# Kernel tuning notes

Measured on AMD Instinct MI355X. Metric: run time of the kernel, lower is better.

The kernel has to match this reference:

```python
import jax, jax.numpy as jnp
import numpy as np

B, NQ, NK = 4, 2048, 2048
DQ = DK = DV = 256
H = 8
HD = DV // H
EPS = 1e-5


def _ln(x, g, b):
    m = jnp.mean(x, axis=-1, keepdims=True)
    v = jnp.mean(jnp.square(x - m), axis=-1, keepdims=True)
    return (x - m) * jax.lax.rsqrt(v + EPS) * g + b


def setup_inputs() -> dict:
    key = jax.random.key(0)
    ks = jax.random.split(key, 12)
    s = 0.02
    return {
        "Q": jax.random.normal(ks[0], (B, NQ, DQ), jnp.float32),
        "K": jax.random.normal(ks[1], (B, NK, DK), jnp.float32),
        "Wq": jax.random.normal(ks[2], (DV, DQ), jnp.float32) * s,
        "bq": jnp.zeros((DV,), jnp.float32),
        "Wk": jax.random.normal(ks[3], (DV, DK), jnp.float32) * s,
        "bk": jnp.zeros((DV,), jnp.float32),
        "Wv": jax.random.normal(ks[4], (DV, DK), jnp.float32) * s,
        "bv": jnp.zeros((DV,), jnp.float32),
        "Wo": jax.random.normal(ks[5], (DV, DV), jnp.float32) * s,
        "bo": jnp.zeros((DV,), jnp.float32),
        "g0": jnp.ones((DV,), jnp.float32),
        "b0": jnp.zeros((DV,), jnp.float32),
        "g1": jnp.ones((DV,), jnp.float32),
        "b1": jnp.zeros((DV,), jnp.float32),
    }


def reference(Q, K, Wq, bq, Wk, bk, Wv, bv, Wo, bo, g0, b0, g1, b1):
    Qp = Q @ Wq.T + bq            # [B,NQ,DV]
    Kp = K @ Wk.T + bk            # [B,NK,DV]
    Vp = K @ Wv.T + bv            # [B,NK,DV]
    # split(head_dim, dim=2) + cat(dim=0) == reshape heads from contiguous channel chunks
    qh = Qp.reshape(B, NQ, H, HD)
    kh = Kp.reshape(B, NK, H, HD)
    vh = Vp.reshape(B, NK, H, HD)
    scores = jnp.einsum("bqhd,bkhd->bhqk", qh, kh) / jnp.sqrt(jnp.float32(HD))
    attn = jax.nn.softmax(scores, axis=-1)          # [B,H,NQ,NK]
    o = jnp.einsum("bhqk,bkhd->bqhd", attn, vh).reshape(B, NQ, DV)
    o = _ln(o, g0, b0)
    out = o + jax.nn.relu(o @ Wo.T + bo)
    out = _ln(out, g1, b1)
    return out
```

## Files before the change

kernel.cpp:

```cpp
#include <hip/hip_runtime.h>
#include <hip/hip_bf16.h>
#include <math.h>

#define DV 256
#define NH 8
#define NB 4
#define NQ 2048
#define NKK 2048

typedef __attribute__((ext_vector_type(8))) short s8v;
typedef __attribute__((ext_vector_type(16))) float fx16;

typedef const __attribute__((address_space(1))) char g1c;
typedef __attribute__((address_space(3))) char l3c;

__device__ __forceinline__ void gl_lds16(const void* g, void* l) {
    __builtin_amdgcn_global_load_lds((g1c*)g, (l3c*)l, 16, 0, 0);
}
__device__ __forceinline__ unsigned cvtpk_bf16(float lo, float hi) {
    unsigned r;
    asm("v_cvt_pk_bf16_f32 %0, %1, %2" : "=v"(r) : "v"(lo), "v"(hi));
    return r;
}
__device__ __forceinline__ ushort f2bf(float x) {
    unsigned u = __builtin_bit_cast(unsigned, x);
    return (ushort)((u + 0x7fffu + ((u >> 16) & 1u)) >> 16);
}
__device__ __forceinline__ float bf2f(ushort h) {
    return __builtin_bit_cast(float, (unsigned)h << 16);
}

__global__ __launch_bounds__(256) void prep_w_k(
    const float* __restrict__ Wq, const float* __restrict__ Wk,
    const float* __restrict__ Wv, const float* __restrict__ Wo,
    ushort* __restrict__ Wf)
{
    const int j = blockIdx.x * 256 + threadIdx.x;
    const int w = j >> 13, c = j & 8191;
    const int bn = c >> 11, s = (c >> 8) & 7, cc = c & 255;
    const int colblk = cc >> 7, ks = (cc >> 6) & 1, g5w = (cc >> 5) & 1, l31w = cc & 31;
    const int col = bn * 64 + colblk * 32 + l31w;
    const int k = s * 32 + ks * 16 + g5w * 8;
    const float* Wsrc = (w == 0) ? Wq : (w == 1) ? Wk : (w == 2) ? Wv : Wo;
    const float* src = Wsrc + (size_t)col * 256 + k;
    float4 a = *(const float4*)src;
    float4 b = *(const float4*)(src + 4);
    uint4 pk;
    pk.x = cvtpk_bf16(a.x, a.y); pk.y = cvtpk_bf16(a.z, a.w);
    pk.z = cvtpk_bf16(b.x, b.y); pk.w = cvtpk_bf16(b.z, b.w);
    *(uint4*)(Wf + (size_t)j * 8) = pk;
}

__global__ __launch_bounds__(256) void gemm_qkv_k(
    const float* __restrict__ Qf, const float* __restrict__ Kf,
    const ushort* __restrict__ Wf,
    const float* __restrict__ bq, const float* __restrict__ bk, const float* __restrict__ bv,
    ushort* __restrict__ Qb, ushort* __restrict__ Kb, ushort* __restrict__ Vt)
{
    __shared__ __align__(16) char lds[2][20480];
    const int t = threadIdx.x, lane = t & 63, wv = t >> 6;
    const int l31 = lane & 31, g5 = lane >> 5;
    const int bm = blockIdx.x, bn = blockIdx.y;
    const int z = blockIdx.z;
    const float* Af = (z == 0) ? Qf : Kf;
    const ushort* WF = Wf + (size_t)z * 65536;
    const float* bias = (z == 0) ? bq : (z == 1) ? bk : bv;

    int arow[4], aoff[4];
#pragma unroll
    for (int k = 0; k < 4; ++k) {
        const int q = k * 256 + t, c = q >> 1, p = q & 1;
        arow[k] = bm * 128 + (c >> 7) * 32 + (c & 31);
        aoff[k] = ((c >> 6) & 1) * 16 + ((c >> 5) & 1) * 8 + p * 4;
    }
    const ushort* wsrc = WF + (size_t)(bn * 8) * 2048 + t * 8;

#pragma unroll
    for (int k = 0; k < 4; ++k)
        gl_lds16(Af + (size_t)arow[k] * 256 + aoff[k],
                 &lds[0][k * 4096 + wv * 1024 + lane * 16]);
    gl_lds16(wsrc, &lds[0][16384 + wv * 1024 + lane * 16]);
    __syncthreads();

    fx16 acc0 = {}, acc1 = {};
    for (int s = 0; s < 8; ++s) {
        const int buf = s & 1;
        if (s + 1 < 8) {
#pragma unroll
            for (int k = 0; k < 4; ++k)
                gl_lds16(Af + (size_t)arow[k] * 256 + (s + 1) * 32 + aoff[k],
                         &lds[buf ^ 1][k * 4096 + wv * 1024 + lane * 16]);
            gl_lds16(wsrc + (s + 1) * 2048, &lds[buf ^ 1][16384 + wv * 1024 + lane * 16]);
        }
        const char* Al = lds[buf];
        const char* Wl = lds[buf] + 16384;
        float4 fa0 = *(const float4*)(Al + (wv * 2 + 0) * 2048 + lane * 32);
        float4 fb0 = *(const float4*)(Al + (wv * 2 + 0) * 2048 + lane * 32 + 16);
        float4 fa1 = *(const float4*)(Al + (wv * 2 + 1) * 2048 + lane * 32);
        float4 fb1 = *(const float4*)(Al + (wv * 2 + 1) * 2048 + lane * 32 + 16);
        union { unsigned u[4]; s8v v; } A0, A1;
        A0.u[0] = cvtpk_bf16(fa0.x, fa0.y); A0.u[1] = cvtpk_bf16(fa0.z, fa0.w);
        A0.u[2] = cvtpk_bf16(fb0.x, fb0.y); A0.u[3] = cvtpk_bf16(fb0.z, fb0.w);
        A1.u[0] = cvtpk_bf16(fa1.x, fa1.y); A1.u[1] = cvtpk_bf16(fa1.z, fa1.w);
        A1.u[2] = cvtpk_bf16(fb1.x, fb1.y); A1.u[3] = cvtpk_bf16(fb1.z, fb1.w);
        s8v b00 = *(const s8v*)(Wl + 0 * 1024 + lane * 16);
        s8v b01 = *(const s8v*)(Wl + 1 * 1024 + lane * 16);
        s8v b10 = *(const s8v*)(Wl + 2 * 1024 + lane * 16);
        s8v b11 = *(const s8v*)(Wl + 3 * 1024 + lane * 16);
        __builtin_amdgcn_s_setprio(1);
        acc0 = __builtin_amdgcn_mfma_f32_32x32x16_bf16(A0.v, b00, acc0, 0, 0, 0);
        acc0 = __builtin_amdgcn_mfma_f32_32x32x16_bf16(A1.v, b01, acc0, 0, 0, 0);
        acc1 = __builtin_amdgcn_mfma_f32_32x32x16_bf16(A0.v, b10, acc1, 0, 0, 0);
        acc1 = __builtin_amdgcn_mfma_f32_32x32x16_bf16(A1.v, b11, acc1, 0, 0, 0);
        __builtin_amdgcn_s_setprio(0);
        __syncthreads();
    }

    const int row_b = bm * 128 + wv * 32;
    const float CE = 0.17677669529663687f * 1.4426950408889634f;
    const float bs0 = bias[bn * 64 + l31];
    const float bs1 = bias[bn * 64 + 32 + l31];
    if (z == 0) {
#pragma unroll
        for (int r = 0; r < 16; ++r) {
            const int row_g = row_b + (r & 3) + 8 * (r >> 2) + 4 * g5;
            Qb[(size_t)row_g * 256 + bn * 64 + l31]      = f2bf((acc0[r] + bs0) * CE);
            Qb[(size_t)row_g * 256 + bn * 64 + 32 + l31] = f2bf((acc1[r] + bs1) * CE);
        }
    } else if (z == 1) {
#pragma unroll
        for (int r = 0; r < 16; ++r) {
            const int row_g = row_b + (r & 3) + 8 * (r >> 2) + 4 * g5;
            Kb[(size_t)row_g * 256 + bn * 64 + l31]      = f2bf(acc0[r] + bs0);
            Kb[(size_t)row_g * 256 + bn * 64 + 32 + l31] = f2bf(acc1[r] + bs1);
        }
    } else {
#pragma unroll
        for (int r = 0; r < 16; ++r) {
            const int row_g = row_b + (r & 3) + 8 * (r >> 2) + 4 * g5;
            const int bb = row_g >> 11, n = row_g & 2047;
            Vt[((size_t)(bb * 8 + bn * 2 + 0) * 32 + l31) * 2048 + n] = f2bf(acc0[r] + bs0);
            Vt[((size_t)(bb * 8 + bn * 2 + 1) * 32 + l31) * 2048 + n] = f2bf(acc1[r] + bs1);
        }
    }
}

__global__ __launch_bounds__(256) void flash_mfma_k(
    const ushort* __restrict__ Qb, const ushort* __restrict__ Kb,
    const ushort* __restrict__ Vt, ushort* __restrict__ Osb, float* __restrict__ L)
{
    __shared__ __align__(16) char lds[2][8192];
    const int t = threadIdx.x;
    const int lane = t & 63, wv = t >> 6;
    const int l31 = lane & 31, g5 = lane >> 5;
    const int qt = blockIdx.x, h = blockIdx.y;
    const int b = blockIdx.z >> 1, sp = blockIdx.z & 1;

    s8v qf0, qf1;
    {
        const ushort* qp = Qb + (((size_t)b * NQ + qt * 128 + wv * 32 + l31) << 8) + h * 32 + g5 * 8;
        qf0 = *(const s8v*)(qp);
        qf1 = *(const s8v*)(qp + 16);
    }
    s8v ones;
#pragma unroll
    for (int j = 0; j < 8; ++j) ones[j] = (short)0x3F80;

    const ushort* ksrc = Kb + (((size_t)b * NKK + sp * 1024 + ((t >> 7) * 32 + (t & 31))) << 8)
                            + h * 32 + ((t >> 6) & 1) * 16 + ((t >> 5) & 1) * 8;
    const ushort* vsrc = Vt + (((size_t)(b * NH + h) * 32 + (t & 31)) << 11) + sp * 1024
                            + (t >> 6) * 16 + ((t >> 5) & 1) * 8;

    fx16 O0 = {}, lsum = {};

    gl_lds16(ksrc, &lds[0][wv * 1024]);
    gl_lds16(vsrc, &lds[0][4096 + wv * 1024]);
    __syncthreads();

    for (int kt = 0; kt < 16; ++kt) {
        const int buf = kt & 1;
        if (kt + 1 < 16) {
            gl_lds16(ksrc + (size_t)(kt + 1) * 64 * DV, &lds[buf ^ 1][wv * 1024]);
            gl_lds16(vsrc + (kt + 1) * 64, &lds[buf ^ 1][4096 + wv * 1024]);
        }
        const char* Kl = lds[buf];
        const char* Vl = lds[buf] + 4096;
        s8v kf00 = *(const s8v*)(Kl + 0 * 1024 + lane * 16);
        s8v kf01 = *(const s8v*)(Kl + 1 * 1024 + lane * 16);
        s8v kf10 = *(const s8v*)(Kl + 2 * 1024 + lane * 16);
        s8v kf11 = *(const s8v*)(Kl + 3 * 1024 + lane * 16);
        s8v vfa[4];
        vfa[0] = *(const s8v*)(Vl + 0 * 1024 + lane * 16);
        vfa[1] = *(const s8v*)(Vl + 1 * 1024 + lane * 16);
        vfa[2] = *(const s8v*)(Vl + 2 * 1024 + lane * 16);
        vfa[3] = *(const s8v*)(Vl + 3 * 1024 + lane * 16);

        fx16 z = {};
        __builtin_amdgcn_s_setprio(1);
        fx16 Sa = __builtin_amdgcn_mfma_f32_32x32x16_bf16(kf00, qf0, z, 0, 0, 0);
        Sa = __builtin_amdgcn_mfma_f32_32x32x16_bf16(kf01, qf1, Sa, 0, 0, 0);
        fx16 Sb = __builtin_amdgcn_mfma_f32_32x32x16_bf16(kf10, qf0, z, 0, 0, 0);
        Sb = __builtin_amdgcn_mfma_f32_32x32x16_bf16(kf11, qf1, Sb, 0, 0, 0);
        __builtin_amdgcn_s_setprio(0);

        float p[32];
#pragma unroll
        for (int i = 0; i < 16; ++i) {
            p[i]      = __builtin_amdgcn_exp2f(Sa[i]);
            p[16 + i] = __builtin_amdgcn_exp2f(Sb[i]);
        }

        __builtin_amdgcn_s_setprio(1);
#pragma unroll
        for (int kt2 = 0; kt2 < 4; ++kt2) {
            const int pb = 8 * kt2;
            auto ra = __builtin_amdgcn_permlane32_swap(
                cvtpk_bf16(p[pb + 0], p[pb + 1]), cvtpk_bf16(p[pb + 4], p[pb + 5]), false, false);
            auto rb = __builtin_amdgcn_permlane32_swap(
                cvtpk_bf16(p[pb + 2], p[pb + 3]), cvtpk_bf16(p[pb + 6], p[pb + 7]), false, false);
            union { unsigned u[4]; s8v v; } pf;
            pf.u[0] = ra[0]; pf.u[1] = rb[0]; pf.u[2] = ra[1]; pf.u[3] = rb[1];
            O0   = __builtin_amdgcn_mfma_f32_32x32x16_bf16(vfa[kt2], pf.v, O0, 0, 0, 0);
            lsum = __builtin_amdgcn_mfma_f32_32x32x16_bf16(ones,    pf.v, lsum, 0, 0, 0);
        }
        __builtin_amdgcn_s_setprio(0);
        __syncthreads();
    }

    {
        const int qrow = qt * 128 + wv * 32 + l31;
        ushort* dst0 = Osb + (size_t)sp * (8192 * 256)
                     + (((size_t)b * NQ + qrow) << 8) + h * 32 + g5 * 4;
#pragma unroll
        for (int rr = 0; rr < 4; ++rr) {
            uint2 w;
            w.x = cvtpk_bf16(O0[4 * rr + 0], O0[4 * rr + 1]);
            w.y = cvtpk_bf16(O0[4 * rr + 2], O0[4 * rr + 3]);
            *(uint2*)(dst0 + 8 * rr) = w;
        }
        if (g5 == 0)
            L[(((size_t)sp * NB + b) * NH + h) * NQ + qrow] = lsum[0];
    }
}

__global__ __launch_bounds__(256) void tail_fused_k(
    const ushort* __restrict__ Osb, const float* __restrict__ L,
    const ushort* __restrict__ Wfo,
    const float* __restrict__ g0, const float* __restrict__ b0,
    const float* __restrict__ bo, const float* __restrict__ g1,
    const float* __restrict__ b1, float* __restrict__ out)
{
    __shared__ __align__(16) char alds[16384];
    __shared__ __align__(16) char wlds[2][16384];
    __shared__ float red[4][32][2];
    __shared__ float par[32][2];
    const int t = threadIdx.x, lane = t & 63, wv = t >> 6;
    const int l31 = lane & 31, g5 = lane >> 5;
    const int row0 = blockIdx.x * 32;

#pragma unroll
    for (int it = 0; it < 4; ++it) {
        const int id = it * 256 + t;
        gl_lds16(Wfo + ((size_t)(id >> 8) * 2048 + (id & 255)) * 8, &wlds[0][id * 16]);
    }

    {
        const int h = lane >> 3;
        const size_t SZS = (size_t)8192 * 256;
        const size_t LS = (size_t)NB * NH * NQ;
        const int aid0 = ((lane >> 3) * 4 + ((lane & 7) >> 1)) * 32;
        const int abyte = (lane & 1) * 8;
        const float4 gv = *(const float4*)(g0 + lane * 4);
        const float4 bv = *(const float4*)(b0 + lane * 4);
#pragma unroll
        for (int ps = 0; ps < 8; ++ps) {
            const int row = ps * 4 + wv;
            const int grow = row0 + row;
            const int b = grow >> 11, q = grow & 2047;
            const size_t lbase = ((size_t)b * NH + h) * NQ + q;
            const float inv = 1.f / (L[lbase] + L[LS + lbase]);
            const size_t off = (size_t)grow * 256 + lane * 4;
            const ushort4 x0 = *(const ushort4*)(Osb + off);
            const ushort4 x1 = *(const ushort4*)(Osb + SZS + off);
            float4 x;
            x.x = (bf2f(x0.x) + bf2f(x1.x)) * inv;
            x.y = (bf2f(x0.y) + bf2f(x1.y)) * inv;
            x.z = (bf2f(x0.z) + bf2f(x1.z)) * inv;
            x.w = (bf2f(x0.w) + bf2f(x1.w)) * inv;
            float s  = (x.x + x.y) + (x.z + x.w);
            float sq = fmaf(x.x, x.x, fmaf(x.y, x.y, fmaf(x.z, x.z, x.w * x.w)));
            for (int o = 32; o; o >>= 1) {
                s  += __shfl_xor(s, o);
                sq += __shfl_xor(sq, o);
            }
            const float mean = s * (1.f / 256.f);
            const float var  = sq * (1.f / 256.f) - mean * mean;
            const float ri   = rsqrtf(var + 1e-5f);
            uint2 p;
            p.x = cvtpk_bf16((x.x - mean) * ri * gv.x + bv.x, (x.y - mean) * ri * gv.y + bv.y);
            p.y = cvtpk_bf16((x.z - mean) * ri * gv.z + bv.z, (x.w - mean) * ri * gv.w + bv.w);
            *(uint2*)(alds + (aid0 + row) * 16 + abyte) = p;
        }
    }
    __syncthreads();

    fx16 acc[2] = {};
    for (int s = 0; s < 8; ++s) {
        const int buf = s & 1;
        if (s + 1 < 8) {
#pragma unroll
            for (int it = 0; it < 4; ++it) {
                const int id = it * 256 + t;
                gl_lds16(Wfo + ((size_t)(id >> 8) * 2048 + (s + 1) * 256 + (id & 255)) * 8,
                         &wlds[buf ^ 1][id * 16]);
            }
        }
        s8v a[2], bf[2][2];
#pragma unroll
        for (int ks = 0; ks < 2; ++ks)
            a[ks] = *(const s8v*)(alds + ((s * 4 + ks * 2 + g5) * 32 + l31) * 16);
#pragma unroll
        for (int ks = 0; ks < 2; ++ks)
#pragma unroll
            for (int ch = 0; ch < 2; ++ch)
                bf[ks][ch] = *(const s8v*)(wlds[buf] + (wv * 256 + ch * 128 + ks * 64 + g5 * 32 + l31) * 16);
        __builtin_amdgcn_s_setprio(1);
#pragma unroll
        for (int ch = 0; ch < 2; ++ch) {
            acc[ch] = __builtin_amdgcn_mfma_f32_32x32x16_bf16(a[0], bf[0][ch], acc[ch], 0, 0, 0);
            acc[ch] = __builtin_amdgcn_mfma_f32_32x32x16_bf16(a[1], bf[1][ch], acc[ch], 0, 0, 0);
        }
        __builtin_amdgcn_s_setprio(0);
        __syncthreads();
    }

    const int cg0 = wv * 64 + l31, cg1 = cg0 + 32;
    const float bo0 = bo[cg0], bo1 = bo[cg1];
    const int s0 = cg0 >> 5, kk0 = cg0 & 31;
    const int s1 = cg1 >> 5, kk1 = cg1 & 31;
    const int coff0 = (s0 * 4 + ((kk0 >> 4) << 1) + ((kk0 >> 3) & 1)) * 32;
    const int coff1 = (s1 * 4 + ((kk1 >> 4) << 1) + ((kk1 >> 3) & 1)) * 32;
    float x[2][16];
#pragma unroll
    for (int r = 0; r < 16; ++r) {
        const int row = (r & 3) + 8 * (r >> 2) + 4 * g5;
        const ushort h0v = *(const ushort*)(alds + ((coff0 + row) << 4) + (kk0 & 7) * 2);
        const ushort h1v = *(const ushort*)(alds + ((coff1 + row) << 4) + (kk1 & 7) * 2);
        const float x0 = bf2f(h0v) + fmaxf(acc[0][r] + bo0, 0.f);
        const float x1 = bf2f(h1v) + fmaxf(acc[1][r] + bo1, 0.f);
        x[0][r] = x0; x[1][r] = x1;
        float sv = x0 + x1;
        float sq = fmaf(x0, x0, x1 * x1);
#pragma unroll
        for (int o = 1; o < 32; o <<= 1) {
            sv += __shfl_xor(sv, o);
            sq += __shfl_xor(sq, o);
        }
        if (l31 == 0) { red[wv][row][0] = sv; red[wv][row][1] = sq; }
    }
    __syncthreads();
    if (t < 32) {
        const float sv = (red[0][t][0] + red[1][t][0]) + (red[2][t][0] + red[3][t][0]);
        const float sq = (red[0][t][1] + red[1][t][1]) + (red[2][t][1] + red[3][t][1]);
        const float mean = sv * (1.f / 256.f);
        const float var  = sq * (1.f / 256.f) - mean * mean;
        par[t][0] = mean;
        par[t][1] = rsqrtf(var + 1e-5f);
    }
    __syncthreads();
    const float g1a = g1[cg0], g1b = g1[cg1];
    const float b1a = b1[cg0], b1b = b1[cg1];
#pragma unroll
    for (int r = 0; r < 16; ++r) {
        const int row = (r & 3) + 8 * (r >> 2) + 4 * g5;
        const float mean = par[row][0], ri = par[row][1];
        out[(size_t)(row0 + row) * 256 + cg0] = (x[0][r] - mean) * ri * g1a + b1a;
        out[(size_t)(row0 + row) * 256 + cg1] = (x[1][r] - mean) * ri * g1b + b1b;
    }
}

extern "C" void kernel_launch(void* const* d_in, const int* in_sizes, int n_in,
                              void* d_out, int out_size, void* d_ws, size_t ws_size,
                              hipStream_t stream) {
    const float* Q  = (const float*)d_in[0];
    const float* K  = (const float*)d_in[1];
    const float* Wq = (const float*)d_in[2];
    const float* bq = (const float*)d_in[3];
    const float* Wk = (const float*)d_in[4];
    const float* bk = (const float*)d_in[5];
    const float* Wv = (const float*)d_in[6];
    const float* bv = (const float*)d_in[7];
    const float* Wo = (const float*)d_in[8];
    const float* bo = (const float*)d_in[9];
    const float* g0 = (const float*)d_in[10];
    const float* b0 = (const float*)d_in[11];
    const float* g1 = (const float*)d_in[12];
    const float* b1 = (const float*)d_in[13];
    float* out = (float*)d_out;

    char* wsb = (char*)d_ws;
    const size_t MB = 1u << 20;
    ushort* Wf  = (ushort*)(wsb + 12 * MB);
    ushort* Qb  = (ushort*)(wsb + 0 * MB);
    ushort* Kb  = (ushort*)(wsb + 4 * MB);
    ushort* Vt  = (ushort*)(wsb + 8 * MB);
    ushort* Osb = (ushort*)(wsb + 13 * MB);
    float*  L   = (float*)(wsb + 21 * MB);

    prep_w_k<<<128, 256, 0, stream>>>(Wq, Wk, Wv, Wo, Wf);
    gemm_qkv_k<<<dim3(64, 4, 3), 256, 0, stream>>>(Q, K, Wf, bq, bk, bv, Qb, Kb, Vt);
    flash_mfma_k<<<dim3(16, 8, 8), 256, 0, stream>>>(Qb, Kb, Vt, Osb, L);
    tail_fused_k<<<256, 256, 0, stream>>>(Osb, L, Wf + 3 * 65536, g0, b0, bo, g1, b1, out);
}
```

Baseline: 72.33 us.

## Drop weight prep kernel, convert fp32 weights in-GEMM, deepen flash K/V pipeline

Result: faster. 70.36 us (-2.7%).

```diff
diff --git a/kernel.cpp b/kernel.cpp
--- a/kernel.cpp
+++ b/kernel.cpp
@@ -30,40 +30,19 @@
     return __builtin_bit_cast(float, (unsigned)h << 16);
 }
 
-__global__ __launch_bounds__(256) void prep_w_k(
-    const float* __restrict__ Wq, const float* __restrict__ Wk,
-    const float* __restrict__ Wv, const float* __restrict__ Wo,
-    ushort* __restrict__ Wf)
-{
-    const int j = blockIdx.x * 256 + threadIdx.x;
-    const int w = j >> 13, c = j & 8191;
-    const int bn = c >> 11, s = (c >> 8) & 7, cc = c & 255;
-    const int colblk = cc >> 7, ks = (cc >> 6) & 1, g5w = (cc >> 5) & 1, l31w = cc & 31;
-    const int col = bn * 64 + colblk * 32 + l31w;
-    const int k = s * 32 + ks * 16 + g5w * 8;
-    const float* Wsrc = (w == 0) ? Wq : (w == 1) ? Wk : (w == 2) ? Wv : Wo;
-    const float* src = Wsrc + (size_t)col * 256 + k;
-    float4 a = *(const float4*)src;
-    float4 b = *(const float4*)(src + 4);
-    uint4 pk;
-    pk.x = cvtpk_bf16(a.x, a.y); pk.y = cvtpk_bf16(a.z, a.w);
-    pk.z = cvtpk_bf16(b.x, b.y); pk.w = cvtpk_bf16(b.z, b.w);
-    *(uint4*)(Wf + (size_t)j * 8) = pk;
-}
-
 __global__ __launch_bounds__(256) void gemm_qkv_k(
     const float* __restrict__ Qf, const float* __restrict__ Kf,
-    const ushort* __restrict__ Wf,
+    const float* __restrict__ Wq, const float* __restrict__ Wk, const float* __restrict__ Wv,
     const float* __restrict__ bq, const float* __restrict__ bk, const float* __restrict__ bv,
     ushort* __restrict__ Qb, ushort* __restrict__ Kb, ushort* __restrict__ Vt)
 {
-    __shared__ __align__(16) char lds[2][20480];
+    __shared__ __align__(16) char lds[2][24576];
     const int t = threadIdx.x, lane = t & 63, wv = t >> 6;
     const int l31 = lane & 31, g5 = lane >> 5;
     const int bm = blockIdx.x, bn = blockIdx.y;
     const int z = blockIdx.z;
     const float* Af = (z == 0) ? Qf : Kf;
-    const ushort* WF = Wf + (size_t)z * 65536;
+    const float* Wz = (z == 0) ? Wq : (z == 1) ? Wk : Wv;
     const float* bias = (z == 0) ? bq : (z == 1) ? bk : bv;
 
     int arow[4], aoff[4];
@@ -73,13 +52,17 @@
         arow[k] = bm * 128 + (c >> 7) * 32 + (c & 31);
         aoff[k] = ((c >> 6) & 1) * 16 + ((c >> 5) & 1) * 8 + p * 4;
     }
-    const ushort* wsrc = WF + (size_t)(bn * 8) * 2048 + t * 8;
+    const int ccq = t >> 1, pq = t & 1;
+    const int wkoff = ((ccq >> 6) & 1) * 16 + ((ccq >> 5) & 1) * 8 + pq * 4;
+    const float* wsrc0 = Wz + (size_t)(bn * 64 + 0 * 32 + (ccq & 31)) * 256 + wkoff;
+    const float* wsrc1 = Wz + (size_t)(bn * 64 + 1 * 32 + (ccq & 31)) * 256 + wkoff;
 
 #pragma unroll
     for (int k = 0; k < 4; ++k)
         gl_lds16(Af + (size_t)arow[k] * 256 + aoff[k],
                  &lds[0][k * 4096 + wv * 1024 + lane * 16]);
-    gl_lds16(wsrc, &lds[0][16384 + wv * 1024 + lane * 16]);
+    gl_lds16(wsrc0, &lds[0][16384 + wv * 1024 + lane * 16]);
+    gl_lds16(wsrc1, &lds[0][20480 + wv * 1024 + lane * 16]);
     __syncthreads();
 
     fx16 acc0 = {}, acc1 = {};
@@ -90,7 +73,8 @@
             for (int k = 0; k < 4; ++k)
                 gl_lds16(Af + (size_t)arow[k] * 256 + (s + 1) * 32 + aoff[k],
                          &lds[buf ^ 1][k * 4096 + wv * 1024 + lane * 16]);
-            gl_lds16(wsrc + (s + 1) * 2048, &lds[buf ^ 1][16384 + wv * 1024 + lane * 16]);
+            gl_lds16(wsrc0 + (s + 1) * 32, &lds[buf ^ 1][16384 + wv * 1024 + lane * 16]);
+            gl_lds16(wsrc1 + (s + 1) * 32, &lds[buf ^ 1][20480 + wv * 1024 + lane * 16]);
         }
         const char* Al = lds[buf];
         const char* Wl = lds[buf] + 16384;
@@ -98,20 +82,25 @@
         float4 fb0 = *(const float4*)(Al + (wv * 2 + 0) * 2048 + lane * 32 + 16);
         float4 fa1 = *(const float4*)(Al + (wv * 2 + 1) * 2048 + lane * 32);
         float4 fb1 = *(const float4*)(Al + (wv * 2 + 1) * 2048 + lane * 32 + 16);
-        union { unsigned u[4]; s8v v; } A0, A1;
+        union { unsigned u[4]; s8v v; } A0, A1, B0, B1, B2, B3;
         A0.u[0] = cvtpk_bf16(fa0.x, fa0.y); A0.u[1] = cvtpk_bf16(fa0.z, fa0.w);
         A0.u[2] = cvtpk_bf16(fb0.x, fb0.y); A0.u[3] = cvtpk_bf16(fb0.z, fb0.w);
         A1.u[0] = cvtpk_bf16(fa1.x, fa1.y); A1.u[1] = cvtpk_bf16(fa1.z, fa1.w);
         A1.u[2] = cvtpk_bf16(fb1.x, fb1.y); A1.u[3] = cvtpk_bf16(fb1.z, fb1.w);
-        s8v b00 = *(const s8v*)(Wl + 0 * 1024 + lane * 16);
-        s8v b01 = *(const s8v*)(Wl + 1 * 1024 + lane * 16);
-        s8v b10 = *(const s8v*)(Wl + 2 * 1024 + lane * 16);
-        s8v b11 = *(const s8v*)(Wl + 3 * 1024 + lane * 16);
+#define QKV_WFRAG(B_, J_)                                                        \
+        {                                                                        \
+            float4 w0 = *(const float4*)(Wl + ((J_) * 64 + lane) * 32);          \
+            float4 w1 = *(const float4*)(Wl + ((J_) * 64 + lane) * 32 + 16);     \
+            B_.u[0] = cvtpk_bf16(w0.x, w0.y); B_.u[1] = cvtpk_bf16(w0.z, w0.w);  \
+            B_.u[2] = cvtpk_bf16(w1.x, w1.y); B_.u[3] = cvtpk_bf16(w1.z, w1.w);  \
+        }
+        QKV_WFRAG(B0, 0) QKV_WFRAG(B1, 1) QKV_WFRAG(B2, 2) QKV_WFRAG(B3, 3)
+#undef QKV_WFRAG
         __builtin_amdgcn_s_setprio(1);
-        acc0 = __builtin_amdgcn_mfma_f32_32x32x16_bf16(A0.v, b00, acc0, 0, 0, 0);
-        acc0 = __builtin_amdgcn_mfma_f32_32x32x16_bf16(A1.v, b01, acc0, 0, 0, 0);
-        acc1 = __builtin_amdgcn_mfma_f32_32x32x16_bf16(A0.v, b10, acc1, 0, 0, 0);
-        acc1 = __builtin_amdgcn_mfma_f32_32x32x16_bf16(A1.v, b11, acc1, 0, 0, 0);
+        acc0 = __builtin_amdgcn_mfma_f32_32x32x16_bf16(A0.v, B0.v, acc0, 0, 0, 0);
+        acc0 = __builtin_amdgcn_mfma_f32_32x32x16_bf16(A1.v, B1.v, acc0, 0, 0, 0);
+        acc1 = __builtin_amdgcn_mfma_f32_32x32x16_bf16(A0.v, B2.v, acc1, 0, 0, 0);
+        acc1 = __builtin_amdgcn_mfma_f32_32x32x16_bf16(A1.v, B3.v, acc1, 0, 0, 0);
         __builtin_amdgcn_s_setprio(0);
         __syncthreads();
     }
@@ -149,7 +138,7 @@
     const ushort* __restrict__ Qb, const ushort* __restrict__ Kb,
     const ushort* __restrict__ Vt, ushort* __restrict__ Osb, float* __restrict__ L)
 {
-    __shared__ __align__(16) char lds[2][8192];
+    __shared__ __align__(16) char lds[32768];
     const int t = threadIdx.x;
     const int lane = t & 63, wv = t >> 6;
     const int l31 = lane & 31, g5 = lane >> 5;
@@ -173,59 +162,78 @@
 
     fx16 O0 = {}, lsum = {};
 
-    gl_lds16(ksrc, &lds[0][wv * 1024]);
-    gl_lds16(vsrc, &lds[0][4096 + wv * 1024]);
+    gl_lds16(ksrc,                 &lds[0 * 4096 + wv * 1024]);
+    gl_lds16(vsrc,                 &lds[16384 + 0 * 4096 + wv * 1024]);
+    gl_lds16(ksrc + 64 * DV,       &lds[1 * 4096 + wv * 1024]);
+    gl_lds16(vsrc + 64,            &lds[16384 + 1 * 4096 + wv * 1024]);
     __syncthreads();
 
-    for (int kt = 0; kt < 16; ++kt) {
-        const int buf = kt & 1;
-        if (kt + 1 < 16) {
-            gl_lds16(ksrc + (size_t)(kt + 1) * 64 * DV, &lds[buf ^ 1][wv * 1024]);
-            gl_lds16(vsrc + (kt + 1) * 64, &lds[buf ^ 1][4096 + wv * 1024]);
-        }
-        const char* Kl = lds[buf];
-        const char* Vl = lds[buf] + 4096;
-        s8v kf00 = *(const s8v*)(Kl + 0 * 1024 + lane * 16);
-        s8v kf01 = *(const s8v*)(Kl + 1 * 1024 + lane * 16);
-        s8v kf10 = *(const s8v*)(Kl + 2 * 1024 + lane * 16);
-        s8v kf11 = *(const s8v*)(Kl + 3 * 1024 + lane * 16);
-        s8v vfa[4];
-        vfa[0] = *(const s8v*)(Vl + 0 * 1024 + lane * 16);
-        vfa[1] = *(const s8v*)(Vl + 1 * 1024 + lane * 16);
-        vfa[2] = *(const s8v*)(Vl + 2 * 1024 + lane * 16);
-        vfa[3] = *(const s8v*)(Vl + 3 * 1024 + lane * 16);
-
-        fx16 z = {};
-        __builtin_amdgcn_s_setprio(1);
-        fx16 Sa = __builtin_amdgcn_mfma_f32_32x32x16_bf16(kf00, qf0, z, 0, 0, 0);
-        Sa = __builtin_amdgcn_mfma_f32_32x32x16_bf16(kf01, qf1, Sa, 0, 0, 0);
-        fx16 Sb = __builtin_amdgcn_mfma_f32_32x32x16_bf16(kf10, qf0, z, 0, 0, 0);
-        Sb = __builtin_amdgcn_mfma_f32_32x32x16_bf16(kf11, qf1, Sb, 0, 0, 0);
-        __builtin_amdgcn_s_setprio(0);
-
-        float p[32];
-#pragma unroll
-        for (int i = 0; i < 16; ++i) {
-            p[i]      = __builtin_amdgcn_exp2f(Sa[i]);
-            p[16 + i] = __builtin_amdgcn_exp2f(Sb[i]);
-        }
-
-        __builtin_amdgcn_s_setprio(1);
-#pragma unroll
-        for (int kt2 = 0; kt2 < 4; ++kt2) {
-            const int pb = 8 * kt2;
-            auto ra = __builtin_amdgcn_permlane32_swap(
-                cvtpk_bf16(p[pb + 0], p[pb + 1]), cvtpk_bf16(p[pb + 4], p[pb + 5]), false, false);
-            auto rb = __builtin_amdgcn_permlane32_swap(
-                cvtpk_bf16(p[pb + 2], p[pb + 3]), cvtpk_bf16(p[pb + 6], p[pb + 7]), false, false);
-            union { unsigned u[4]; s8v v; } pf;
-            pf.u[0] = ra[0]; pf.u[1] = rb[0]; pf.u[2] = ra[1]; pf.u[3] = rb[1];
-            O0   = __builtin_amdgcn_mfma_f32_32x32x16_bf16(vfa[kt2], pf.v, O0, 0, 0, 0);
-            lsum = __builtin_amdgcn_mfma_f32_32x32x16_bf16(ones,    pf.v, lsum, 0, 0, 0);
-        }
-        __builtin_amdgcn_s_setprio(0);
+#define FLASH_TILE(SLOT)                                                                           \
+    do {                                                                                           \
+        const char* Kl = lds + (SLOT) * 4096;                                                      \
+        const char* Vl = lds + 16384 + (SLOT) * 4096;                                              \
+        s8v kf00 = *(const s8v*)(Kl + 0 * 1024 + lane * 16);                                       \
+        s8v kf01 = *(const s8v*)(Kl + 1 * 1024 + lane * 16);                                       \
+        s8v kf10 = *(const s8v*)(Kl + 2 * 1024 + lane * 16);                                       \
+        s8v kf11 = *(const s8v*)(Kl + 3 * 1024 + lane * 16);                                       \
+        s8v vfa[4];                                                                                \
+        vfa[0] = *(const s8v*)(Vl + 0 * 1024 + lane * 16);                                         \
+        vfa[1] = *(const s8v*)(Vl + 1 * 1024 + lane * 16);                                         \
+        vfa[2] = *(const s8v*)(Vl + 2 * 1024 + lane * 16);                                         \
+        vfa[3] = *(const s8v*)(Vl + 3 * 1024 + lane * 16);                                         \
+        fx16 zz = {};                                                                              \
+        __builtin_amdgcn_s_setprio(1);                                                             \
+        fx16 Sa = __builtin_amdgcn_mfma_f32_32x32x16_bf16(kf00, qf0, zz, 0, 0, 0);                 \
+        Sa = __builtin_amdgcn_mfma_f32_32x32x16_bf16(kf01, qf1, Sa, 0, 0, 0);                      \
+        fx16 Sb = __builtin_amdgcn_mfma_f32_32x32x16_bf16(kf10, qf0, zz, 0, 0, 0);                 \
+        Sb = __builtin_amdgcn_mfma_f32_32x32x16_bf16(kf11, qf1, Sb, 0, 0, 0);                      \
+        __builtin_amdgcn_s_setprio(0);                                                             \
+        float pa[16];                                                                              \
+        _Pragma("unroll")                                                                          \
+        for (int i = 0; i < 16; ++i) pa[i] = __builtin_amdgcn_exp2f(Sa[i]);                        \
+        _Pragma("unroll")                                                                          \
+        for (int kt2 = 0; kt2 < 2; ++kt2) {                                                        \
+            const int pb = 8 * kt2;                                                                \
+            auto ra = __builtin_amdgcn_permlane32_swap(                                            \
+                cvtpk_bf16(pa[pb + 0], pa[pb + 1]), cvtpk_bf16(pa[pb + 4], pa[pb + 5]), false, false); \
+            auto rb = __builtin_amdgcn_permlane32_swap(                                            \
+                cvtpk_bf16(pa[pb + 2], pa[pb + 3]), cvtpk_bf16(pa[pb + 6], pa[pb + 7]), false, false); \
+            union { unsigned u[4]; s8v v; } pf;                                                    \
+            pf.u[0] = ra[0]; pf.u[1] = rb[0]; pf.u[2] = ra[1]; pf.u[3] = rb[1];                    \
+            O0   = __builtin_amdgcn_mfma_f32_32x32x16_bf16(vfa[kt2], pf.v, O0, 0, 0, 0);           \
+            lsum = __builtin_amdgcn_mfma_f32_32x32x16_bf16(ones,    pf.v, lsum, 0, 0, 0);          \
+        }                                                                                          \
+        float pb2[16];                                                                             \
+        _Pragma("unroll")                                                                          \
+        for (int i = 0; i < 16; ++i) pb2[i] = __builtin_amdgcn_exp2f(Sb[i]);                       \
+        _Pragma("unroll")                                                                          \
+        for (int kt2 = 2; kt2 < 4; ++kt2) {                                                        \
+            const int pb = 8 * (kt2 - 2);                                                          \
+            auto ra = __builtin_amdgcn_permlane32_swap(                                            \
+                cvtpk_bf16(pb2[pb + 0], pb2[pb + 1]), cvtpk_bf16(pb2[pb + 4], pb2[pb + 5]), false, false); \
+            auto rb = __builtin_amdgcn_permlane32_swap(                                            \
+                cvtpk_bf16(pb2[pb + 2], pb2[pb + 3]), cvtpk_bf16(pb2[pb + 6], pb2[pb + 7]), false, false); \
+            union { unsigned u[4]; s8v v; } pf;                                                    \
+            pf.u[0] = ra[0]; pf.u[1] = rb[0]; pf.u[2] = ra[1]; pf.u[3] = rb[1];                    \
+            O0   = __builtin_amdgcn_mfma_f32_32x32x16_bf16(vfa[kt2], pf.v, O0, 0, 0, 0);           \
+            lsum = __builtin_amdgcn_mfma_f32_32x32x16_bf16(ones,    pf.v, lsum, 0, 0, 0);          \
+        }                                                                                          \
+    } while (0)
+
+    for (int it2 = 0; it2 < 8; ++it2) {
+        const int ta = 2 * it2;
+        if (it2 < 7) {
+            const int sA = (ta + 2) & 3, sB = (ta + 3) & 3;
+            gl_lds16(ksrc + (size_t)(ta + 2) * 64 * DV, &lds[sA * 4096 + wv * 1024]);
+            gl_lds16(vsrc + (ta + 2) * 64,              &lds[16384 + sA * 4096 + wv * 1024]);
+            gl_lds16(ksrc + (size_t)(ta + 3) * 64 * DV, &lds[sB * 4096 + wv * 1024]);
+            gl_lds16(vsrc + (ta + 3) * 64,              &lds[16384 + sB * 4096 + wv * 1024]);
+        }
+        FLASH_TILE(ta & 3);
+        FLASH_TILE((ta + 1) & 3);
         __syncthreads();
     }
+#undef FLASH_TILE
 
     {
         const int qrow = qt * 128 + wv * 32 + l31;
@@ -245,24 +253,30 @@
 
 __global__ __launch_bounds__(256) void tail_fused_k(
     const ushort* __restrict__ Osb, const float* __restrict__ L,
-    const ushort* __restrict__ Wfo,
+    const float* __restrict__ Wo,
     const float* __restrict__ g0, const float* __restrict__ b0,
     const float* __restrict__ bo, const float* __restrict__ g1,
     const float* __restrict__ b1, float* __restrict__ out)
 {
     __shared__ __align__(16) char alds[16384];
-    __shared__ __align__(16) char wlds[2][16384];
+    __shared__ __align__(16) char wlds[2][32768];
     __shared__ float red[4][32][2];
     __shared__ float par[32][2];
     const int t = threadIdx.x, lane = t & 63, wv = t >> 6;
     const int l31 = lane & 31, g5 = lane >> 5;
     const int row0 = blockIdx.x * 32;
 
-#pragma unroll
-    for (int it = 0; it < 4; ++it) {
-        const int id = it * 256 + t;
-        gl_lds16(Wfo + ((size_t)(id >> 8) * 2048 + (id & 255)) * 8, &wlds[0][id * 16]);
-    }
+    const int ccq = t >> 1, pq = t & 1;
+    const int wkoff = ((ccq >> 6) & 1) * 16 + ((ccq >> 5) & 1) * 8 + pq * 4;
+    const int colb = ccq & 31;
+#define TAIL_WSTAGE(BUF, S)                                                            \
+    _Pragma("unroll")                                                                  \
+    for (int i = 0; i < 8; ++i) {                                                      \
+        const int col = (i >> 1) * 64 + (i & 1) * 32 + colb;                           \
+        gl_lds16(Wo + (size_t)col * 256 + (S) * 32 + wkoff,                            \
+                 &wlds[BUF][i * 4096 + wv * 1024 + lane * 16]);                        \
+    }
+    TAIL_WSTAGE(0, 0)
 
     {
         const int h = lane >> 3;
@@ -308,31 +322,35 @@
     for (int s = 0; s < 8; ++s) {
         const int buf = s & 1;
         if (s + 1 < 8) {
-#pragma unroll
-            for (int it = 0; it < 4; ++it) {
-                const int id = it * 256 + t;
-                gl_lds16(Wfo + ((size_t)(id >> 8) * 2048 + (s + 1) * 256 + (id & 255)) * 8,
-                         &wlds[buf ^ 1][id * 16]);
-            }
-        }
-        s8v a[2], bf[2][2];
+            TAIL_WSTAGE(buf ^ 1, s + 1)
+        }
+        s8v a[2];
 #pragma unroll
         for (int ks = 0; ks < 2; ++ks)
             a[ks] = *(const s8v*)(alds + ((s * 4 + ks * 2 + g5) * 32 + l31) * 16);
+        union { unsigned u[4]; s8v v; } bf[2][2];
 #pragma unroll
         for (int ks = 0; ks < 2; ++ks)
 #pragma unroll
-            for (int ch = 0; ch < 2; ++ch)
-                bf[ks][ch] = *(const s8v*)(wlds[buf] + (wv * 256 + ch * 128 + ks * 64 + g5 * 32 + l31) * 16);
+            for (int ch = 0; ch < 2; ++ch) {
+                const int id = wv * 256 + ch * 128 + ks * 64 + g5 * 32 + l31;
+                float4 w0 = *(const float4*)(wlds[buf] + id * 32);
+                float4 w1 = *(const float4*)(wlds[buf] + id * 32 + 16);
+                bf[ks][ch].u[0] = cvtpk_bf16(w0.x, w0.y);
+                bf[ks][ch].u[1] = cvtpk_bf16(w0.z, w0.w);
+                bf[ks][ch].u[2] = cvtpk_bf16(w1.x, w1.y);
+                bf[ks][ch].u[3] = cvtpk_bf16(w1.z, w1.w);
+            }
         __builtin_amdgcn_s_setprio(1);
 #pragma unroll
         for (int ch = 0; ch < 2; ++ch) {
-            acc[ch] = __builtin_amdgcn_mfma_f32_32x32x16_bf16(a[0], bf[0][ch], acc[ch], 0, 0, 0);
-            acc[ch] = __builtin_amdgcn_mfma_f32_32x32x16_bf16(a[1], bf[1][ch], acc[ch], 0, 0, 0);
+            acc[ch] = __builtin_amdgcn_mfma_f32_32x32x16_bf16(a[0], bf[0][ch].v, acc[ch], 0, 0, 0);
+            acc[ch] = __builtin_amdgcn_mfma_f32_32x32x16_bf16(a[1], bf[1][ch].v, acc[ch], 0, 0, 0);
         }
         __builtin_amdgcn_s_setprio(0);
         __syncthreads();
     }
+#undef TAIL_WSTAGE
 
     const int cg0 = wv * 64 + l31, cg1 = cg0 + 32;
     const float bo0 = bo[cg0], bo1 = bo[cg1];
@@ -400,15 +418,13 @@
 
     char* wsb = (char*)d_ws;
     const size_t MB = 1u << 20;
-    ushort* Wf  = (ushort*)(wsb + 12 * MB);
     ushort* Qb  = (ushort*)(wsb + 0 * MB);
     ushort* Kb  = (ushort*)(wsb + 4 * MB);
     ushort* Vt  = (ushort*)(wsb + 8 * MB);
     ushort* Osb = (ushort*)(wsb + 13 * MB);
     float*  L   = (float*)(wsb + 21 * MB);
 
-    prep_w_k<<<128, 256, 0, stream>>>(Wq, Wk, Wv, Wo, Wf);
-    gemm_qkv_k<<<dim3(64, 4, 3), 256, 0, stream>>>(Q, K, Wf, bq, bk, bv, Qb, Kb, Vt);
+    gemm_qkv_k<<<dim3(64, 4, 3), 256, 0, stream>>>(Q, K, Wq, Wk, Wv, bq, bk, bv, Qb, Kb, Vt);
     flash_mfma_k<<<dim3(16, 8, 8), 256, 0, stream>>>(Qb, Kb, Vt, Osb, L);
-    tail_fused_k<<<256, 256, 0, stream>>>(Osb, L, Wf + 3 * 65536, g0, b0, bo, g1, b1, out);
-}
+    tail_fused_k<<<256, 256, 0, stream>>>(Osb, L, Wo, g0, b0, bo, g1, b1, out);
+}
```
